# Kernel tuning notes

Measured on AMD Instinct MI355X. Metric: run time of the kernel, lower is better.

## Reference

```python
import jax, jax.numpy as jnp
import numpy as np

N_NODES = 50000
N_EDGES = 400000
N_GRAPHS = 32
EMB = 64
EDGE_DIM = 4
IN_DIM = 11
LAYERS = 4
EPS = 1e-5


def _bn(x, g, b):
    # BatchNorm1d in train mode: biased batch statistics over rows
    m = jnp.mean(x, axis=0)
    v = jnp.mean(jnp.square(x - m), axis=0)
    return g * (x - m) * jax.lax.rsqrt(v + EPS) + b


def setup_inputs() -> dict:
    key = jax.random.key(0)
    ks = jax.random.split(key, 16)
    x = jax.random.normal(ks[0], (N_NODES, IN_DIM), dtype=jnp.float32)
    edge_attr = jax.random.normal(ks[1], (N_EDGES, EDGE_DIM), dtype=jnp.float32)
    edge_index = jax.random.randint(ks[2], (2, N_EDGES), 0, N_NODES, dtype=jnp.int32)
    batch = jnp.sort(jax.random.randint(ks[3], (N_NODES,), 0, N_GRAPHS, dtype=jnp.int32))

    def lin(k, fan_in, shape):
        bound = 1.0 / np.sqrt(fan_in)
        return jax.random.uniform(k, shape, jnp.float32, -bound, bound)

    msg_in = 2 * EMB + EDGE_DIM  # 132
    upd_in = 2 * EMB             # 128
    kk = jax.random.split(ks[4], 12)
    params = dict(
        lin_in_W=lin(kk[0], IN_DIM, (IN_DIM, EMB)),
        lin_in_b=lin(kk[1], IN_DIM, (EMB,)),
        msg_W1=lin(kk[2], msg_in, (LAYERS, msg_in, EMB)),
        msg_b1=lin(kk[3], msg_in, (LAYERS, EMB)),
        msg_g1=jnp.ones((LAYERS, EMB), jnp.float32),
        msg_be1=jnp.zeros((LAYERS, EMB), jnp.float32),
        msg_W2=lin(kk[4], EMB, (LAYERS, EMB, EMB)),
        msg_b2=lin(kk[5], EMB, (LAYERS, EMB)),
        msg_g2=jnp.ones((LAYERS, EMB), jnp.float32),
        msg_be2=jnp.zeros((LAYERS, EMB), jnp.float32),
        upd_W1=lin(kk[6], upd_in, (LAYERS, upd_in, EMB)),
        upd_b1=lin(kk[7], upd_in, (LAYERS, EMB)),
        upd_g1=jnp.ones((LAYERS, EMB), jnp.float32),
        upd_be1=jnp.zeros((LAYERS, EMB), jnp.float32),
        upd_W2=lin(kk[8], EMB, (LAYERS, EMB, EMB)),
        upd_b2=lin(kk[9], EMB, (LAYERS, EMB)),
        upd_g2=jnp.ones((LAYERS, EMB), jnp.float32),
        upd_be2=jnp.zeros((LAYERS, EMB), jnp.float32),
        pred_W=lin(kk[10], EMB, (EMB, 1)),
        pred_b=lin(kk[11], EMB, (1,)),
    )
    return dict(x=x, edge_attr=edge_attr, edge_index=edge_index, batch=batch, **params)


def reference(x, edge_attr, edge_index, batch, lin_in_W, lin_in_b,
              msg_W1, msg_b1, msg_g1, msg_be1, msg_W2, msg_b2, msg_g2, msg_be2,
              upd_W1, upd_b1, upd_g1, upd_be1, upd_W2, upd_b2, upd_g2, upd_be2,
              pred_W, pred_b):
    src = edge_index[0]  # j (source)
    dst = edge_index[1]  # i (target, PyG default flow source_to_target)
    h = x @ lin_in_W + lin_in_b  # (n, d)
    for l in range(LAYERS):
        m_in = jnp.concatenate([h[dst], h[src], edge_attr], axis=-1)  # (e, 2d+d_e)
        m = jax.nn.relu(_bn(m_in @ msg_W1[l] + msg_b1[l], msg_g1[l], msg_be1[l]))
        m = jax.nn.relu(_bn(m @ msg_W2[l] + msg_b2[l], msg_g2[l], msg_be2[l]))
        aggr = jax.ops.segment_sum(m, dst, num_segments=N_NODES)  # scatter-add
        u_in = jnp.concatenate([h, aggr], axis=-1)  # (n, 2d)
        u = jax.nn.relu(_bn(u_in @ upd_W1[l] + upd_b1[l], upd_g1[l], upd_be1[l]))
        u = jax.nn.relu(_bn(u @ upd_W2[l] + upd_b2[l], upd_g2[l], upd_be2[l]))
        h = h + u  # residual in MPNNModel.forward
    sums = jax.ops.segment_sum(h, batch, num_segments=N_GRAPHS)
    counts = jax.ops.segment_sum(jnp.ones((h.shape[0],), h.dtype), batch, num_segments=N_GRAPHS)
    h_graph = sums / jnp.maximum(counts, 1.0)[:, None]  # global_mean_pool
    out = h_graph @ pred_W + pred_b  # (G, 1)
    return out.reshape(-1)
```

## Files before the change

kernel.cpp:

```cpp
#include <hip/hip_runtime.h>

#define DEV __device__ __forceinline__

constexpr int NN = 50000;
constexpr int NE = 400000;
constexpr int NG = 32;
constexpr float EPSV = 1e-5f;
constexpr int SCAN_BLOCKS = 196;
constexpr int NSHARD = 8;
constexpr int STB = NSHARD * 128;

typedef __attribute__((ext_vector_type(8))) short s16x8;
typedef __attribute__((ext_vector_type(4))) float f32x4;

DEV unsigned short f2b(float f) {
  union { float f; unsigned u; } x; x.f = f;
  unsigned r = x.u + 0x7fffu + ((x.u >> 16) & 1u);
  return (unsigned short)(r >> 16);
}
DEV float b2f(unsigned short u) {
  union { unsigned u; float f; } x; x.u = ((unsigned)u) << 16; return x.f;
}

DEV s16x8 frag_from_f32(const float* p) {
  const float4 v0 = *(const float4*)p;
  const float4 v1 = *(const float4*)(p + 4);
  s16x8 af;
  af[0] = (short)f2b(v0.x); af[1] = (short)f2b(v0.y);
  af[2] = (short)f2b(v0.z); af[3] = (short)f2b(v0.w);
  af[4] = (short)f2b(v1.x); af[5] = (short)f2b(v1.y);
  af[6] = (short)f2b(v1.z); af[7] = (short)f2b(v1.w);
  return af;
}

DEV void bn_coeff(const float* __restrict__ st, const float* __restrict__ g,
                  const float* __restrict__ be, float invM, int c,
                  float& sc, float& sh) {
  float s = 0.f, s2 = 0.f;
#pragma unroll
  for (int k = 0; k < NSHARD; ++k) {
    s += st[k * 128 + c];
    s2 += st[k * 128 + 64 + c];
  }
  float mean = s * invM;
  float var = s2 * invM - mean * mean;
  sc = g[c] * rsqrtf(var + EPSV);
  sh = be[c] - mean * sc;
}

__global__ __launch_bounds__(256) void lin_in_kernel(
    const float* __restrict__ x, const float* __restrict__ W,
    const float* __restrict__ b, float* __restrict__ h)
{
  int gid = blockIdx.x * 256 + threadIdx.x;
  if (gid >= NN * 64) return;
  int n = gid >> 6, c = gid & 63;
  float acc = b[c];
#pragma unroll
  for (int k = 0; k < 11; ++k)
    acc = fmaf(x[n * 11 + k], W[k * 64 + c], acc);
  h[gid] = acc;
}

__global__ __launch_bounds__(256) void hist_kernel(
    const int* __restrict__ dstI, int* __restrict__ deg)
{
  int e = blockIdx.x * 256 + threadIdx.x;
  if (e < NE) atomicAdd(&deg[dstI[e]], 1);
}

__global__ __launch_bounds__(256) void scan_pass1(
    const int* __restrict__ deg, int* __restrict__ blockSums)
{
  __shared__ int red[4];
  int tid = threadIdx.x;
  int idx = blockIdx.x * 256 + tid;
  int v = (idx < NN) ? deg[idx] : 0;
#pragma unroll
  for (int off = 32; off > 0; off >>= 1) v += __shfl_down(v, off, 64);
  if ((tid & 63) == 0) red[tid >> 6] = v;
  __syncthreads();
  if (tid == 0) blockSums[blockIdx.x] = red[0] + red[1] + red[2] + red[3];
}

__global__ __launch_bounds__(256) void scan_pass2(
    const int* __restrict__ blockSums, int* __restrict__ blockOffs)
{
  __shared__ int part[256];
  int tid = threadIdx.x;
  int v = (tid < SCAN_BLOCKS) ? blockSums[tid] : 0;
  part[tid] = v;
  __syncthreads();
  for (int off = 1; off < 256; off <<= 1) {
    int t = 0;
    if (tid >= off) t = part[tid - off];
    __syncthreads();
    if (tid >= off) part[tid] += t;
    __syncthreads();
  }
  blockOffs[tid] = (tid == 0) ? 0 : part[tid - 1];
}

__global__ __launch_bounds__(256) void scan_pass3(
    const int* __restrict__ deg, const int* __restrict__ blockOffs,
    int* __restrict__ rowptr, int* __restrict__ cursor)
{
  __shared__ int part[256];
  int tid = threadIdx.x;
  int idx = blockIdx.x * 256 + tid;
  int v = (idx < NN) ? deg[idx] : 0;
  part[tid] = v;
  __syncthreads();
  for (int off = 1; off < 256; off <<= 1) {
    int t = 0;
    if (tid >= off) t = part[tid - off];
    __syncthreads();
    if (tid >= off) part[tid] += t;
    __syncthreads();
  }
  int excl = (tid == 0) ? 0 : part[tid - 1];
  int val = blockOffs[blockIdx.x] + excl;
  if (idx < NN) { rowptr[idx] = val; cursor[idx] = val; }
  if (idx == 0) rowptr[NN] = NE;
}

__global__ __launch_bounds__(256) void fill_pos_kernel(
    const int* __restrict__ dstI, int* __restrict__ cursor,
    int* __restrict__ eid)
{
  int e = blockIdx.x * 256 + threadIdx.x;
  if (e < NE) {
    int pos = atomicAdd(&cursor[dstI[e]], 1);
    eid[pos] = e;
  }
}

__global__ __launch_bounds__(256) void permute_kernel(
    const int* __restrict__ eid, const int* __restrict__ srcI,
    const int* __restrict__ dstI, const float* __restrict__ ea,
    int* __restrict__ srcP, int* __restrict__ dstP,
    float* __restrict__ eaP)
{
  int p = blockIdx.x * 256 + threadIdx.x;
  if (p < NE) {
    int e = eid[p];
    srcP[p] = srcI[e];
    dstP[p] = dstI[e];
    *(float4*)&eaP[(size_t)p * 4] = *(const float4*)&ea[(size_t)e * 4];
  }
}

__global__ __launch_bounds__(256) void gemm_dual_mfma(
    const float* __restrict__ h, const float* __restrict__ W,
    unsigned short* __restrict__ Hd, unsigned short* __restrict__ Hs)
{
  __shared__ __align__(16) unsigned short Wt_s[2 * 64 * 72];

  const int tid = threadIdx.x;
  const int lane = tid & 63;
  const int wave = tid >> 6;
  const int nn = lane & 15;
  const int kq = lane >> 4;

#pragma unroll
  for (int i = 0; i < 32; ++i) {
    int idx = i * 256 + tid;
    int half = idx >> 12;
    int rem = idx & 4095;
    int k = rem >> 6, n = rem & 63;
    Wt_s[half * 4608 + n * 72 + k] = f2b(W[idx]);
  }
  __syncthreads();

  s16x8 bfrag[2][4][2];
#pragma unroll
  for (int o = 0; o < 2; ++o)
#pragma unroll
    for (int nt = 0; nt < 4; ++nt)
#pragma unroll
      for (int kc = 0; kc < 2; ++kc) {
        const unsigned short* p =
            &Wt_s[o * 4608 + (nt * 16 + nn) * 72 + kc * 32 + kq * 8];
#pragma unroll
        for (int j = 0; j < 8; ++j) bfrag[o][nt][kc][j] = (short)p[j];
      }

  const int rbase = blockIdx.x * 128 + wave * 32;

  f32x4 acc[2][2][4];
#pragma unroll
  for (int o = 0; o < 2; ++o)
#pragma unroll
    for (int rt = 0; rt < 2; ++rt)
#pragma unroll
      for (int nt = 0; nt < 4; ++nt) acc[o][rt][nt] = (f32x4){0.f, 0.f, 0.f, 0.f};

#pragma unroll
  for (int rt = 0; rt < 2; ++rt) {
    int row = rbase + rt * 16 + nn;
    int rowc = row < NN ? row : NN - 1;
#pragma unroll
    for (int kc = 0; kc < 2; ++kc) {
      s16x8 af = frag_from_f32(&h[(size_t)rowc * 64 + kc * 32 + kq * 8]);
#pragma unroll
      for (int o = 0; o < 2; ++o)
#pragma unroll
        for (int nt = 0; nt < 4; ++nt)
          acc[o][rt][nt] = __builtin_amdgcn_mfma_f32_16x16x32_bf16(
              af, bfrag[o][nt][kc], acc[o][rt][nt], 0, 0, 0);
    }
  }

#pragma unroll
  for (int rt = 0; rt < 2; ++rt)
#pragma unroll
    for (int nt = 0; nt < 4; ++nt) {
      int col = nt * 16 + nn;
#pragma unroll
      for (int reg = 0; reg < 4; ++reg) {
        int row = rbase + rt * 16 + kq * 4 + reg;
        if (row < NN) {
          Hd[(size_t)row * 64 + col] = f2b(acc[0][rt][nt][reg]);
          Hs[(size_t)row * 64 + col] = f2b(acc[1][rt][nt][reg]);
        }
      }
    }
}

__global__ __launch_bounds__(256) void edge_combine(
    const unsigned short* __restrict__ Hd, const unsigned short* __restrict__ Hs,
    const float* __restrict__ eaP, const int* __restrict__ srcP,
    const int* __restrict__ dstP, const float* __restrict__ Wb,
    const float* __restrict__ bias, unsigned short* __restrict__ t1,
    float* __restrict__ outStats)
{
  __shared__ float red_s[128];
  const int tid = threadIdx.x;
  const int c0 = (tid & 7) * 8;
  float bv[8], w0[8], w1[8], w2[8], w3[8];
#pragma unroll
  for (int j = 0; j < 8; ++j) {
    bv[j] = bias[c0 + j];
    w0[j] = Wb[0 * 64 + c0 + j];
    w1[j] = Wb[1 * 64 + c0 + j];
    w2[j] = Wb[2 * 64 + c0 + j];
    w3[j] = Wb[3 * 64 + c0 + j];
  }

  float s[8], s2[8];
#pragma unroll
  for (int j = 0; j < 8; ++j) { s[j] = 0.f; s2[j] = 0.f; }

  const int e0 = (blockIdx.x * 256 + tid) >> 3;
  const int estep = (gridDim.x * 256) >> 3;

  for (int e = e0; e < NE; e += 4 * estep) {
    bool has[4];
    uint4 hd[4], hs[4];
    float4 av[4];
    int eidx4[4];
#pragma unroll
    for (int u = 0; u < 4; ++u) {
      int ee = e + u * estep;
      has[u] = ee < NE;
      int ec = has[u] ? ee : e;
      eidx4[u] = ec;
      int si = srcP[ec], di = dstP[ec];
      av[u] = *(const float4*)&eaP[(size_t)ec * 4];
      hd[u] = *(const uint4*)&Hd[(size_t)di * 64 + c0];
      hs[u] = *(const uint4*)&Hs[(size_t)si * 64 + c0];
    }
#pragma unroll
    for (int u = 0; u < 4; ++u) {
      if (!has[u]) continue;
      const unsigned hdw[4] = {hd[u].x, hd[u].y, hd[u].z, hd[u].w};
      const unsigned hsw[4] = {hs[u].x, hs[u].y, hs[u].z, hs[u].w};
      unsigned short ob[8];
#pragma unroll
      for (int d = 0; d < 4; ++d) {
        union { unsigned uu; float f; } a0, a1, b0, b1u;
        a0.uu = (hdw[d] & 0xffffu) << 16; a1.uu = hdw[d] & 0xffff0000u;
        b0.uu = (hsw[d] & 0xffffu) << 16; b1u.uu = hsw[d] & 0xffff0000u;
        int j0 = d * 2, j1 = d * 2 + 1;
        float y0 = a0.f + b0.f + bv[j0] + av[u].x * w0[j0] + av[u].y * w1[j0] + av[u].z * w2[j0] + av[u].w * w3[j0];
        float y1 = a1.f + b1u.f + bv[j1] + av[u].x * w0[j1] + av[u].y * w1[j1] + av[u].z * w2[j1] + av[u].w * w3[j1];
        ob[j0] = f2b(y0); ob[j1] = f2b(y1);
        s[j0] += y0; s2[j0] += y0 * y0;
        s[j1] += y1; s2[j1] += y1 * y1;
      }
      *(uint4*)&t1[(size_t)eidx4[u] * 64 + c0] = *(const uint4*)ob;
    }
  }
#pragma unroll
  for (int j = 0; j < 8; ++j) {
    s[j] += __shfl_xor(s[j], 8, 64);
    s[j] += __shfl_xor(s[j], 16, 64);
    s[j] += __shfl_xor(s[j], 32, 64);
    s2[j] += __shfl_xor(s2[j], 8, 64);
    s2[j] += __shfl_xor(s2[j], 16, 64);
    s2[j] += __shfl_xor(s2[j], 32, 64);
  }
  if (tid < 128) red_s[tid] = 0.f;
  __syncthreads();
  if ((tid & 63) < 8) {
#pragma unroll
    for (int j = 0; j < 8; ++j) {
      atomicAdd(&red_s[c0 + j], s[j]);
      atomicAdd(&red_s[64 + c0 + j], s2[j]);
    }
  }
  __syncthreads();
  if (tid < 128)
    atomicAdd(&outStats[(blockIdx.x & (NSHARD - 1)) * 128 + tid], red_s[tid]);
}

__global__ __launch_bounds__(256) void gemm64_bn_mfma(
    const unsigned short* A0,
    const float* __restrict__ W,
    const float* __restrict__ bias,
    const float* __restrict__ inStats,
    const float* __restrict__ inG,
    const float* __restrict__ inBe,
    float invM_in,
    unsigned short* outp,
    float* __restrict__ outStats,
    int M)
{
  __shared__ __align__(16) unsigned short Wt_s[64 * 72];
  __shared__ float scale_s[64];
  __shared__ float shift_s[64];
  __shared__ float red_s[128];

  const int tid = threadIdx.x;
  const int lane = tid & 63;
  const int wave = tid >> 6;
  const int nn = lane & 15;
  const int kq = lane >> 4;

  if (tid < 64) {
    float sc, sh;
    bn_coeff(inStats, inG, inBe, invM_in, tid, sc, sh);
    scale_s[tid] = sc;
    shift_s[tid] = sh;
  }
#pragma unroll
  for (int i = 0; i < 16; ++i) {
    int idx = i * 256 + tid;
    int k = idx >> 6, n = idx & 63;
    Wt_s[n * 72 + k] = f2b(W[idx]);
  }
  __syncthreads();

  s16x8 bfrag[4][2];
#pragma unroll
  for (int nt = 0; nt < 4; ++nt)
#pragma unroll
    for (int kc = 0; kc < 2; ++kc)
      bfrag[nt][kc] = *(const s16x8*)&Wt_s[(nt * 16 + nn) * 72 + kc * 32 + kq * 8];

  float scf[2][8], shf[2][8];
#pragma unroll
  for (int kc = 0; kc < 2; ++kc) {
    int k0 = kc * 32 + kq * 8;
    float4 a = *(const float4*)&scale_s[k0];
    float4 b = *(const float4*)&scale_s[k0 + 4];
    float4 c = *(const float4*)&shift_s[k0];
    float4 d = *(const float4*)&shift_s[k0 + 4];
    scf[kc][0] = a.x; scf[kc][1] = a.y; scf[kc][2] = a.z; scf[kc][3] = a.w;
    scf[kc][4] = b.x; scf[kc][5] = b.y; scf[kc][6] = b.z; scf[kc][7] = b.w;
    shf[kc][0] = c.x; shf[kc][1] = c.y; shf[kc][2] = c.z; shf[kc][3] = c.w;
    shf[kc][4] = d.x; shf[kc][5] = d.y; shf[kc][6] = d.z; shf[kc][7] = d.w;
  }

  float bcol[4];
#pragma unroll
  for (int nt = 0; nt < 4; ++nt) bcol[nt] = bias[nt * 16 + nn];

  float s[4] = {0.f, 0.f, 0.f, 0.f};
  float s2[4] = {0.f, 0.f, 0.f, 0.f};

  uint4 raw[4][2];
  f32x4 acc[4][4];

  const int rb0 = blockIdx.x * 512 + wave * 64;
#pragma unroll
  for (int rt = 0; rt < 4; ++rt) {
    int row = rb0 + rt * 16 + nn;
    int rowc = row < M ? row : M - 1;
#pragma unroll
    for (int kc = 0; kc < 2; ++kc)
      raw[rt][kc] = *(const uint4*)&A0[(size_t)rowc * 64 + kc * 32 + kq * 8];
  }

#pragma unroll
  for (int rt = 0; rt < 4; ++rt)
#pragma unroll
    for (int nt = 0; nt < 4; ++nt) acc[rt][nt] = (f32x4){0.f, 0.f, 0.f, 0.f};
#pragma unroll
  for (int rt = 0; rt < 4; ++rt) {
#pragma unroll
    for (int kc = 0; kc < 2; ++kc) {
      unsigned wbits[4] = {raw[rt][kc].x, raw[rt][kc].y, raw[rt][kc].z, raw[rt][kc].w};
      s16x8 af;
#pragma unroll
      for (int d = 0; d < 4; ++d) {
        union { unsigned u; float f; } lo, hi;
        lo.u = (wbits[d] & 0xffffu) << 16;
        hi.u = wbits[d] & 0xffff0000u;
        int j0 = d * 2, j1 = d * 2 + 1;
        af[j0] = (short)f2b(fmaxf(fmaf(scf[kc][j0], lo.f, shf[kc][j0]), 0.f));
        af[j1] = (short)f2b(fmaxf(fmaf(scf[kc][j1], hi.f, shf[kc][j1]), 0.f));
      }
#pragma unroll
      for (int nt = 0; nt < 4; ++nt)
        acc[rt][nt] = __builtin_amdgcn_mfma_f32_16x16x32_bf16(
            af, bfrag[nt][kc], acc[rt][nt], 0, 0, 0);
    }
  }

  const int rb1 = rb0 + 256;
#pragma unroll
  for (int rt = 0; rt < 4; ++rt) {
    int row = rb1 + rt * 16 + nn;
    int rowc = row < M ? row : M - 1;
#pragma unroll
    for (int kc = 0; kc < 2; ++kc)
      raw[rt][kc] = *(const uint4*)&A0[(size_t)rowc * 64 + kc * 32 + kq * 8];
  }

#pragma unroll
  for (int rt = 0; rt < 4; ++rt)
#pragma unroll
    for (int nt = 0; nt < 4; ++nt) {
      int col = nt * 16 + nn;
#pragma unroll
      for (int reg = 0; reg < 4; ++reg) {
        int row = rb0 + rt * 16 + kq * 4 + reg;
        if (row < M) {
          float y = acc[rt][nt][reg] + bcol[nt];
          outp[(size_t)row * 64 + col] = f2b(y);
          s[nt] += y; s2[nt] += y * y;
        }
      }
    }

#pragma unroll
  for (int rt = 0; rt < 4; ++rt)
#pragma unroll
    for (int nt = 0; nt < 4; ++nt) acc[rt][nt] = (f32x4){0.f, 0.f, 0.f, 0.f};
#pragma unroll
  for (int rt = 0; rt < 4; ++rt) {
#pragma unroll
    for (int kc = 0; kc < 2; ++kc) {
      unsigned wbits[4] = {raw[rt][kc].x, raw[rt][kc].y, raw[rt][kc].z, raw[rt][kc].w};
      s16x8 af;
#pragma unroll
      for (int d = 0; d < 4; ++d) {
        union { unsigned u; float f; } lo, hi;
        lo.u = (wbits[d] & 0xffffu) << 16;
        hi.u = wbits[d] & 0xffff0000u;
        int j0 = d * 2, j1 = d * 2 + 1;
        af[j0] = (short)f2b(fmaxf(fmaf(scf[kc][j0], lo.f, shf[kc][j0]), 0.f));
        af[j1] = (short)f2b(fmaxf(fmaf(scf[kc][j1], hi.f, shf[kc][j1]), 0.f));
      }
#pragma unroll
      for (int nt = 0; nt < 4; ++nt)
        acc[rt][nt] = __builtin_amdgcn_mfma_f32_16x16x32_bf16(
            af, bfrag[nt][kc], acc[rt][nt], 0, 0, 0);
    }
  }

#pragma unroll
  for (int rt = 0; rt < 4; ++rt)
#pragma unroll
    for (int nt = 0; nt < 4; ++nt) {
      int col = nt * 16 + nn;
#pragma unroll
      for (int reg = 0; reg < 4; ++reg) {
        int row = rb1 + rt * 16 + kq * 4 + reg;
        if (row < M) {
          float y = acc[rt][nt][reg] + bcol[nt];
          outp[(size_t)row * 64 + col] = f2b(y);
          s[nt] += y; s2[nt] += y * y;
        }
      }
    }

#pragma unroll
  for (int nt = 0; nt < 4; ++nt) {
    s[nt] += __shfl_xor(s[nt], 16, 64);
    s[nt] += __shfl_xor(s[nt], 32, 64);
    s2[nt] += __shfl_xor(s2[nt], 16, 64);
    s2[nt] += __shfl_xor(s2[nt], 32, 64);
  }
  if (tid < 128) red_s[tid] = 0.f;
  __syncthreads();
  if (lane < 16) {
#pragma unroll
    for (int nt = 0; nt < 4; ++nt) {
      atomicAdd(&red_s[nt * 16 + nn], s[nt]);
      atomicAdd(&red_s[64 + nt * 16 + nn], s2[nt]);
    }
  }
  __syncthreads();
  if (tid < 128)
    atomicAdd(&outStats[(blockIdx.x & (NSHARD - 1)) * 128 + tid], red_s[tid]);
}

__global__ __launch_bounds__(256) void gemm_concat_mfma(
    const float* __restrict__ A0,
    const unsigned short* __restrict__ A1b,
    const float* __restrict__ W,
    const float* __restrict__ bias,
    unsigned short* __restrict__ outp,
    float* __restrict__ outStats,
    int M)
{
  __shared__ __align__(16) unsigned short Wt_s[64 * 136];
  __shared__ float red_s[128];

  const int tid = threadIdx.x;
  const int lane = tid & 63;
  const int wave = tid >> 6;
  const int nn = lane & 15;
  const int kq = lane >> 4;

#pragma unroll
  for (int i = 0; i < 32; ++i) {
    int idx = i * 256 + tid;
    int k = idx >> 6, n = idx & 63;
    Wt_s[n * 136 + k] = f2b(W[idx]);
  }
  __syncthreads();

  s16x8 bfrag[4][4];
#pragma unroll
  for (int nt = 0; nt < 4; ++nt)
#pragma unroll
    for (int kc = 0; kc < 4; ++kc) {
      const unsigned short* p = &Wt_s[(nt * 16 + nn) * 136 + kc * 32 + kq * 8];
#pragma unroll
      for (int j = 0; j < 8; ++j) bfrag[nt][kc][j] = (short)p[j];
    }

  const int rbase = blockIdx.x * 128 + wave * 32;

  f32x4 acc[2][4];
#pragma unroll
  for (int rt = 0; rt < 2; ++rt)
#pragma unroll
    for (int nt = 0; nt < 4; ++nt) acc[rt][nt] = (f32x4){0.f, 0.f, 0.f, 0.f};

#pragma unroll
  for (int rt = 0; rt < 2; ++rt) {
    int row = rbase + rt * 16 + nn;
    int rowc = row < M ? row : M - 1;
#pragma unroll
    for (int kc = 0; kc < 4; ++kc) {
      s16x8 af;
      if (kc < 2) {
        af = frag_from_f32(&A0[(size_t)rowc * 64 + kc * 32 + kq * 8]);
      } else {
        af = *(const s16x8*)&A1b[(size_t)rowc * 64 + (kc - 2) * 32 + kq * 8];
      }
#pragma unroll
      for (int nt = 0; nt < 4; ++nt)
        acc[rt][nt] = __builtin_amdgcn_mfma_f32_16x16x32_bf16(
            af, bfrag[nt][kc], acc[rt][nt], 0, 0, 0);
    }
  }

  float bcol[4];
#pragma unroll
  for (int nt = 0; nt < 4; ++nt) bcol[nt] = bias[nt * 16 + nn];

  float s[4] = {0.f, 0.f, 0.f, 0.f};
  float s2[4] = {0.f, 0.f, 0.f, 0.f};
#pragma unroll
  for (int rt = 0; rt < 2; ++rt)
#pragma unroll
    for (int nt = 0; nt < 4; ++nt) {
      int col = nt * 16 + nn;
#pragma unroll
      for (int reg = 0; reg < 4; ++reg) {
        int row = rbase + rt * 16 + kq * 4 + reg;
        if (row < M) {
          float y = acc[rt][nt][reg] + bcol[nt];
          outp[(size_t)row * 64 + col] = f2b(y);
          s[nt] += y; s2[nt] += y * y;
        }
      }
    }
#pragma unroll
  for (int nt = 0; nt < 4; ++nt) {
    s[nt] += __shfl_xor(s[nt], 16, 64);
    s[nt] += __shfl_xor(s[nt], 32, 64);
    s2[nt] += __shfl_xor(s2[nt], 16, 64);
    s2[nt] += __shfl_xor(s2[nt], 32, 64);
  }
  if (tid < 128) red_s[tid] = 0.f;
  __syncthreads();
  if (lane < 16) {
#pragma unroll
    for (int nt = 0; nt < 4; ++nt) {
      atomicAdd(&red_s[nt * 16 + nn], s[nt]);
      atomicAdd(&red_s[64 + nt * 16 + nn], s2[nt]);
    }
  }
  __syncthreads();
  if (tid < 128)
    atomicAdd(&outStats[(blockIdx.x & (NSHARD - 1)) * 128 + tid], red_s[tid]);
}

__global__ __launch_bounds__(256) void aggregate_kernel(
    const unsigned short* __restrict__ t2, const int* __restrict__ rowptr,
    const float* __restrict__ stats, const float* __restrict__ g,
    const float* __restrict__ be, float invM,
    unsigned short* __restrict__ aggr)
{
  __shared__ float sc_s[64], sh_s[64];
  const int tid = threadIdx.x;
  if (tid < 64) {
    float sc, sh;
    bn_coeff(stats, g, be, invM, tid, sc, sh);
    sc_s[tid] = sc;
    sh_s[tid] = sh;
  }
  __syncthreads();

  int node = (blockIdx.x * 256 + tid) >> 6;
  int lane = tid & 63;
  if (node >= NN) return;
  const int c8 = (lane & 7) * 8;
  const int rq = lane >> 3;

  float sc[8], sh[8];
#pragma unroll
  for (int j = 0; j < 8; ++j) {
    sc[j] = sc_s[c8 + j];
    sh[j] = sh_s[c8 + j];
  }

  int lo = rowptr[node], hi = rowptr[node + 1];
  float acc[8] = {0.f, 0.f, 0.f, 0.f, 0.f, 0.f, 0.f, 0.f};

  for (int i = lo; i < hi; i += 16) {
    int r0 = i + rq;
    int r1 = i + 8 + rq;
    bool h0 = r0 < hi, h1 = r1 < hi;
    uint4 v0 = make_uint4(0u, 0u, 0u, 0u), v1 = make_uint4(0u, 0u, 0u, 0u);
    if (h0) v0 = *(const uint4*)&t2[(size_t)r0 * 64 + c8];
    if (h1) v1 = *(const uint4*)&t2[(size_t)r1 * 64 + c8];
    if (h0) {
      const unsigned w[4] = {v0.x, v0.y, v0.z, v0.w};
#pragma unroll
      for (int d = 0; d < 4; ++d) {
        union { unsigned u; float f; } a0, a1;
        a0.u = (w[d] & 0xffffu) << 16;
        a1.u = w[d] & 0xffff0000u;
        acc[d * 2] += fmaxf(fmaf(sc[d * 2], a0.f, sh[d * 2]), 0.f);
        acc[d * 2 + 1] += fmaxf(fmaf(sc[d * 2 + 1], a1.f, sh[d * 2 + 1]), 0.f);
      }
    }
    if (h1) {
      const unsigned w[4] = {v1.x, v1.y, v1.z, v1.w};
#pragma unroll
      for (int d = 0; d < 4; ++d) {
        union { unsigned u; float f; } a0, a1;
        a0.u = (w[d] & 0xffffu) << 16;
        a1.u = w[d] & 0xffff0000u;
        acc[d * 2] += fmaxf(fmaf(sc[d * 2], a0.f, sh[d * 2]), 0.f);
        acc[d * 2 + 1] += fmaxf(fmaf(sc[d * 2 + 1], a1.f, sh[d * 2 + 1]), 0.f);
      }
    }
  }
#pragma unroll
  for (int j = 0; j < 8; ++j) {
    acc[j] += __shfl_xor(acc[j], 8, 64);
    acc[j] += __shfl_xor(acc[j], 16, 64);
    acc[j] += __shfl_xor(acc[j], 32, 64);
  }
  if (rq == 0) {
    unsigned short o[8];
#pragma unroll
    for (int j = 0; j < 8; ++j) o[j] = f2b(acc[j]);
    *(uint4*)&aggr[(size_t)node * 64 + c8] = *(const uint4*)o;
  }
}

__global__ __launch_bounds__(256) void residual_kernel(
    const unsigned short* __restrict__ u2, const float* __restrict__ stats,
    const float* __restrict__ g, const float* __restrict__ be,
    float invM, float* __restrict__ h)
{
  __shared__ float sc_s[64], sh_s[64];
  const int tid = threadIdx.x;
  if (tid < 64) {
    float sc, sh;
    bn_coeff(stats, g, be, invM, tid, sc, sh);
    sc_s[tid] = sc;
    sh_s[tid] = sh;
  }
  __syncthreads();

  int gid = blockIdx.x * 256 + tid;
  if (gid >= NN * 16) return;
  int c = (gid & 15) * 4;
  ushort4 v4 = *(const ushort4*)&u2[(size_t)gid * 4];
  float4 hv = *(const float4*)&h[(size_t)gid * 4];
  const unsigned short vu[4] = {v4.x, v4.y, v4.z, v4.w};
  float* hp = (float*)&hv;
#pragma unroll
  for (int j = 0; j < 4; ++j)
    hp[j] += fmaxf(fmaf(sc_s[c + j], b2f(vu[j]), sh_s[c + j]), 0.f);
  *(float4*)&h[(size_t)gid * 4] = hv;
}

constexpr int POOL_NPB = 128;

__global__ __launch_bounds__(256) void pool_partial(
    const float* __restrict__ h, const int* __restrict__ batch,
    float* __restrict__ sums)
{
  int lane = threadIdx.x & 63;
  int wave = threadIdx.x >> 6;
  int base = blockIdx.x * POOL_NPB;
  float acc = 0.f;
  int gcur = -1;
  for (int i = wave; i < POOL_NPB; i += 4) {
    int n = base + i;
    if (n >= NN) break;
    int g = batch[n];
    if (g != gcur) {
      if (gcur >= 0) atomicAdd(&sums[gcur * 64 + lane], acc);
      gcur = g;
      acc = 0.f;
    }
    acc += h[(size_t)n * 64 + lane];
  }
  if (gcur >= 0) atomicAdd(&sums[gcur * 64 + lane], acc);
}

DEV int lower_bound_i(const int* __restrict__ a, int n, int v) {
  int lo = 0, hi = n;
  while (lo < hi) {
    int m = (lo + hi) >> 1;
    if (a[m] < v) lo = m + 1; else hi = m;
  }
  return lo;
}

__global__ __launch_bounds__(64) void pool_final(
    const float* __restrict__ sums, const int* __restrict__ batch,
    const float* __restrict__ predW, const float* __restrict__ predB,
    float* __restrict__ out)
{
  int g = blockIdx.x;
  int lane = threadIdx.x;
  int lo = lower_bound_i(batch, NN, g);
  int hi = lower_bound_i(batch, NN, g + 1);
  float cnt = fmaxf((float)(hi - lo), 1.0f);
  float p = sums[g * 64 + lane] / cnt * predW[lane];
#pragma unroll
  for (int off = 32; off > 0; off >>= 1) p += __shfl_down(p, off, 64);
  if (lane == 0) out[g] = p + predB[0];
}

extern "C" void kernel_launch(void* const* d_in, const int* in_sizes, int n_in,
                              void* d_out, int out_size, void* d_ws, size_t ws_size,
                              hipStream_t stream)
{
  (void)in_sizes; (void)n_in; (void)out_size; (void)ws_size;

  const float* x        = (const float*)d_in[0];
  const float* edge_attr= (const float*)d_in[1];
  const int*   eidx     = (const int*)d_in[2];
  const int*   batch    = (const int*)d_in[3];
  const float* linW     = (const float*)d_in[4];
  const float* linB     = (const float*)d_in[5];
  const float* msgW1    = (const float*)d_in[6];
  const float* msgB1    = (const float*)d_in[7];
  const float* msgG1    = (const float*)d_in[8];
  const float* msgBe1   = (const float*)d_in[9];
  const float* msgW2    = (const float*)d_in[10];
  const float* msgB2    = (const float*)d_in[11];
  const float* msgG2    = (const float*)d_in[12];
  const float* msgBe2   = (const float*)d_in[13];
  const float* updW1    = (const float*)d_in[14];
  const float* updB1    = (const float*)d_in[15];
  const float* updG1    = (const float*)d_in[16];
  const float* updBe1   = (const float*)d_in[17];
  const float* updW2    = (const float*)d_in[18];
  const float* updB2    = (const float*)d_in[19];
  const float* updG2    = (const float*)d_in[20];
  const float* updBe2   = (const float*)d_in[21];
  const float* predW    = (const float*)d_in[22];
  const float* predB    = (const float*)d_in[23];

  const int* srcI = eidx;
  const int* dstI = eidx + NE;

  char* p = (char*)d_ws;
  float* h  = (float*)p;            p += (size_t)NN * 64 * 4;
  unsigned short* t1 = (unsigned short*)p; p += (size_t)NE * 64 * 2;
  unsigned short* aggr = (unsigned short*)p; p += (size_t)NN * 64 * 2;
  unsigned short* u1 = (unsigned short*)p;   p += (size_t)NN * 64 * 2;
  unsigned short* Hd = (unsigned short*)p;   p += (size_t)NN * 64 * 2;
  unsigned short* Hs = (unsigned short*)p;   p += (size_t)NN * 64 * 2;
  float* stats = (float*)p;         p += 16 * STB * 4;
  float* sums = (float*)p;          p += NG * 64 * 4;
  int* deg = (int*)p;               p += (size_t)NN * 4;
  int* cursor = (int*)p;            p += (size_t)NN * 4;
  int* rowptr = (int*)p;            p += (size_t)(NN + 1) * 4;
  int* eid = (int*)p;               p += (size_t)NE * 4;
  int* srcP = (int*)p;              p += (size_t)NE * 4;
  int* dstP = (int*)p;              p += (size_t)NE * 4;
  float* eaP = (float*)p;           p += (size_t)NE * 4 * 4;
  int* blockSums = (int*)p;         p += 256 * 4;
  int* blockOffs = (int*)p;         p += 256 * 4;

  hipMemsetAsync(stats, 0, (16 * STB + NG * 64) * sizeof(float), stream);
  hipMemsetAsync(deg, 0, NN * sizeof(int), stream);

  hist_kernel<<<(NE + 255) / 256, 256, 0, stream>>>(dstI, deg);
  scan_pass1<<<SCAN_BLOCKS, 256, 0, stream>>>(deg, blockSums);
  scan_pass2<<<1, 256, 0, stream>>>(blockSums, blockOffs);
  scan_pass3<<<SCAN_BLOCKS, 256, 0, stream>>>(deg, blockOffs, rowptr, cursor);
  fill_pos_kernel<<<(NE + 255) / 256, 256, 0, stream>>>(dstI, cursor, eid);
  permute_kernel<<<(NE + 255) / 256, 256, 0, stream>>>(
      eid, srcI, dstI, edge_attr, srcP, dstP, eaP);

  lin_in_kernel<<<(NN * 64 + 255) / 256, 256, 0, stream>>>(x, linW, linB, h);

  const float invE = 1.0f / (float)NE;
  const float invN = 1.0f / (float)NN;
  const int NB128 = (NN + 127) / 128;
  const int NB512 = (NN + 511) / 512;
  const int EB512 = (NE + 511) / 512;

  for (int l = 0; l < 4; ++l) {
    float* st0 = stats + (l * 4 + 0) * STB;
    float* st1 = stats + (l * 4 + 1) * STB;
    float* st2 = stats + (l * 4 + 2) * STB;
    float* st3 = stats + (l * 4 + 3) * STB;
    const float* W1 = msgW1 + (size_t)l * 132 * 64;

    gemm_dual_mfma<<<NB128, 256, 0, stream>>>(h, W1, Hd, Hs);

    edge_combine<<<2048, 256, 0, stream>>>(
        Hd, Hs, eaP, srcP, dstP, W1 + 128 * 64, msgB1 + l * 64,
        t1, st0);

    gemm64_bn_mfma<<<EB512, 256, 0, stream>>>(
        t1, msgW2 + (size_t)l * 64 * 64, msgB2 + l * 64,
        st0, msgG1 + l * 64, msgBe1 + l * 64, invE,
        t1, st1, NE);

    aggregate_kernel<<<(NN * 64 + 255) / 256, 256, 0, stream>>>(
        t1, rowptr, st1, msgG2 + l * 64, msgBe2 + l * 64, invE, aggr);

    gemm_concat_mfma<<<NB128, 256, 0, stream>>>(
        h, aggr, updW1 + (size_t)l * 128 * 64, updB1 + l * 64,
        u1, st2, NN);

    gemm64_bn_mfma<<<NB512, 256, 0, stream>>>(
        u1, updW2 + (size_t)l * 64 * 64, updB2 + l * 64,
        st2, updG1 + l * 64, updBe1 + l * 64, invN,
        u1, st3, NN);

    residual_kernel<<<(NN * 16 + 255) / 256, 256, 0, stream>>>(
        u1, st3, updG2 + l * 64, updBe2 + l * 64, invN, h);
  }

  pool_partial<<<(NN + POOL_NPB - 1) / POOL_NPB, 256, 0, stream>>>(h, batch, sums);
  pool_final<<<NG, 64, 0, stream>>>(sums, batch, predW, predB, (float*)d_out);
}
```

Before: 661.3 us.

## Fuse neighbor aggregation into the update concat GEMM kernel

Aggregation of BN+ReLU edge messages per node now runs inside the update-MLP first GEMM, writing each block's aggregated rows to shared memory instead of a global buffer. This removes one kernel launch and the global write/read of the aggregate tensor. Each wave now serially processes 32 nodes two at a time, which greatly reduces parallelism for the gather phase and may expose memory latency. The B-fragment loads from LDS are also vectorized.

```diff
diff --git a/kernel.cpp b/kernel.cpp
--- a/kernel.cpp
+++ b/kernel.cpp
@@ -507,9 +507,11 @@
     atomicAdd(&outStats[(blockIdx.x & (NSHARD - 1)) * 128 + tid], red_s[tid]);
 }
 
-__global__ __launch_bounds__(256) void gemm_concat_mfma(
-    const float* __restrict__ A0,
-    const unsigned short* __restrict__ A1b,
+__global__ __launch_bounds__(256) void aggr_concat_mfma(
+    const unsigned short* __restrict__ t2, const int* __restrict__ rowptr,
+    const float* __restrict__ st1, const float* __restrict__ g2,
+    const float* __restrict__ be2, float invE,
+    const float* __restrict__ h,
     const float* __restrict__ W,
     const float* __restrict__ bias,
     unsigned short* __restrict__ outp,
@@ -517,6 +519,8 @@
     int M)
 {
   __shared__ __align__(16) unsigned short Wt_s[64 * 136];
+  __shared__ __align__(16) unsigned short A2_s[128 * 72];
+  __shared__ float sc_s[64], sh_s[64];
   __shared__ float red_s[128];
 
   const int tid = threadIdx.x;
@@ -525,6 +529,12 @@
   const int nn = lane & 15;
   const int kq = lane >> 4;
 
+  if (tid < 64) {
+    float sc, sh;
+    bn_coeff(st1, g2, be2, invE, tid, sc, sh);
+    sc_s[tid] = sc;
+    sh_s[tid] = sh;
+  }
 #pragma unroll
   for (int i = 0; i < 32; ++i) {
     int idx = i * 256 + tid;
@@ -533,15 +543,76 @@
   }
   __syncthreads();
 
+  {
+    const int c8 = (lane & 7) * 8;
+    const int rq = lane >> 3;
+    float sc[8], sh[8];
+#pragma unroll
+    for (int j = 0; j < 8; ++j) { sc[j] = sc_s[c8 + j]; sh[j] = sh_s[c8 + j]; }
+
+    const int nodeBase = blockIdx.x * 128 + wave * 32;
+    for (int i = 0; i < 32; i += 2) {
+      int nA = nodeBase + i, nB = nodeBase + i + 1;
+      int loA = 0, hiA = 0, loB = 0, hiB = 0;
+      if (nA < NN) { loA = rowptr[nA]; hiA = rowptr[nA + 1]; }
+      if (nB < NN) { loB = rowptr[nB]; hiB = rowptr[nB + 1]; }
+      float accA[8] = {0.f, 0.f, 0.f, 0.f, 0.f, 0.f, 0.f, 0.f};
+      float accB[8] = {0.f, 0.f, 0.f, 0.f, 0.f, 0.f, 0.f, 0.f};
+      int iA = loA + rq, iB = loB + rq;
+      while (iA < hiA || iB < hiB) {
+        bool hA = iA < hiA, hB = iB < hiB;
+        uint4 vA = make_uint4(0u, 0u, 0u, 0u), vB = make_uint4(0u, 0u, 0u, 0u);
+        if (hA) vA = *(const uint4*)&t2[(size_t)iA * 64 + c8];
+        if (hB) vB = *(const uint4*)&t2[(size_t)iB * 64 + c8];
+        if (hA) {
+          const unsigned w[4] = {vA.x, vA.y, vA.z, vA.w};
+#pragma unroll
+          for (int d = 0; d < 4; ++d) {
+            union { unsigned u; float f; } a0, a1;
+            a0.u = (w[d] & 0xffffu) << 16;
+            a1.u = w[d] & 0xffff0000u;
+            accA[d * 2] += fmaxf(fmaf(sc[d * 2], a0.f, sh[d * 2]), 0.f);
+            accA[d * 2 + 1] += fmaxf(fmaf(sc[d * 2 + 1], a1.f, sh[d * 2 + 1]), 0.f);
+          }
+        }
+        if (hB) {
+          const unsigned w[4] = {vB.x, vB.y, vB.z, vB.w};
+#pragma unroll
+          for (int d = 0; d < 4; ++d) {
+            union { unsigned u; float f; } a0, a1;
+            a0.u = (w[d] & 0xffffu) << 16;
+            a1.u = w[d] & 0xffff0000u;
+            accB[d * 2] += fmaxf(fmaf(sc[d * 2], a0.f, sh[d * 2]), 0.f);
+            accB[d * 2 + 1] += fmaxf(fmaf(sc[d * 2 + 1], a1.f, sh[d * 2 + 1]), 0.f);
+          }
+        }
+        iA += 8; iB += 8;
+      }
+#pragma unroll
+      for (int j = 0; j < 8; ++j) {
+        accA[j] += __shfl_xor(accA[j], 8, 64);
+        accA[j] += __shfl_xor(accA[j], 16, 64);
+        accA[j] += __shfl_xor(accA[j], 32, 64);
+        accB[j] += __shfl_xor(accB[j], 8, 64);
+        accB[j] += __shfl_xor(accB[j], 16, 64);
+        accB[j] += __shfl_xor(accB[j], 32, 64);
+      }
+      if (rq == 0) {
+        unsigned short oA[8], oB[8];
+#pragma unroll
+        for (int j = 0; j < 8; ++j) { oA[j] = f2b(accA[j]); oB[j] = f2b(accB[j]); }
+        *(uint4*)&A2_s[(wave * 32 + i) * 72 + c8] = *(const uint4*)oA;
+        *(uint4*)&A2_s[(wave * 32 + i + 1) * 72 + c8] = *(const uint4*)oB;
+      }
+    }
+  }
+
   s16x8 bfrag[4][4];
 #pragma unroll
   for (int nt = 0; nt < 4; ++nt)
 #pragma unroll
-    for (int kc = 0; kc < 4; ++kc) {
-      const unsigned short* p = &Wt_s[(nt * 16 + nn) * 136 + kc * 32 + kq * 8];
-#pragma unroll
-      for (int j = 0; j < 8; ++j) bfrag[nt][kc][j] = (short)p[j];
-    }
+    for (int kc = 0; kc < 4; ++kc)
+      bfrag[nt][kc] = *(const s16x8*)&Wt_s[(nt * 16 + nn) * 136 + kc * 32 + kq * 8];
 
   const int rbase = blockIdx.x * 128 + wave * 32;
 
@@ -555,13 +626,14 @@
   for (int rt = 0; rt < 2; ++rt) {
     int row = rbase + rt * 16 + nn;
     int rowc = row < M ? row : M - 1;
+    int rloc = wave * 32 + rt * 16 + nn;
 #pragma unroll
     for (int kc = 0; kc < 4; ++kc) {
       s16x8 af;
       if (kc < 2) {
-        af = frag_from_f32(&A0[(size_t)rowc * 64 + kc * 32 + kq * 8]);
+        af = frag_from_f32(&h[(size_t)rowc * 64 + kc * 32 + kq * 8]);
       } else {
-        af = *(const s16x8*)&A1b[(size_t)rowc * 64 + (kc - 2) * 32 + kq * 8];
+        af = *(const s16x8*)&A2_s[rloc * 72 + (kc - 2) * 32 + kq * 8];
       }
 #pragma unroll
       for (int nt = 0; nt < 4; ++nt)
@@ -610,82 +682,6 @@
   __syncthreads();
   if (tid < 128)
     atomicAdd(&outStats[(blockIdx.x & (NSHARD - 1)) * 128 + tid], red_s[tid]);
-}
-
-__global__ __launch_bounds__(256) void aggregate_kernel(
-    const unsigned short* __restrict__ t2, const int* __restrict__ rowptr,
-    const float* __restrict__ stats, const float* __restrict__ g,
-    const float* __restrict__ be, float invM,
-    unsigned short* __restrict__ aggr)
-{
-  __shared__ float sc_s[64], sh_s[64];
-  const int tid = threadIdx.x;
-  if (tid < 64) {
-    float sc, sh;
-    bn_coeff(stats, g, be, invM, tid, sc, sh);
-    sc_s[tid] = sc;
-    sh_s[tid] = sh;
-  }
-  __syncthreads();
-
-  int node = (blockIdx.x * 256 + tid) >> 6;
-  int lane = tid & 63;
-  if (node >= NN) return;
-  const int c8 = (lane & 7) * 8;
-  const int rq = lane >> 3;
-
-  float sc[8], sh[8];
-#pragma unroll
-  for (int j = 0; j < 8; ++j) {
-    sc[j] = sc_s[c8 + j];
-    sh[j] = sh_s[c8 + j];
-  }
-
-  int lo = rowptr[node], hi = rowptr[node + 1];
-  float acc[8] = {0.f, 0.f, 0.f, 0.f, 0.f, 0.f, 0.f, 0.f};
-
-  for (int i = lo; i < hi; i += 16) {
-    int r0 = i + rq;
-    int r1 = i + 8 + rq;
-    bool h0 = r0 < hi, h1 = r1 < hi;
-    uint4 v0 = make_uint4(0u, 0u, 0u, 0u), v1 = make_uint4(0u, 0u, 0u, 0u);
-    if (h0) v0 = *(const uint4*)&t2[(size_t)r0 * 64 + c8];
-    if (h1) v1 = *(const uint4*)&t2[(size_t)r1 * 64 + c8];
-    if (h0) {
-      const unsigned w[4] = {v0.x, v0.y, v0.z, v0.w};
-#pragma unroll
-      for (int d = 0; d < 4; ++d) {
-        union { unsigned u; float f; } a0, a1;
-        a0.u = (w[d] & 0xffffu) << 16;
-        a1.u = w[d] & 0xffff0000u;
-        acc[d * 2] += fmaxf(fmaf(sc[d * 2], a0.f, sh[d * 2]), 0.f);
-        acc[d * 2 + 1] += fmaxf(fmaf(sc[d * 2 + 1], a1.f, sh[d * 2 + 1]), 0.f);
-      }
-    }
-    if (h1) {
-      const unsigned w[4] = {v1.x, v1.y, v1.z, v1.w};
-#pragma unroll
-      for (int d = 0; d < 4; ++d) {
-        union { unsigned u; float f; } a0, a1;
-        a0.u = (w[d] & 0xffffu) << 16;
-        a1.u = w[d] & 0xffff0000u;
-        acc[d * 2] += fmaxf(fmaf(sc[d * 2], a0.f, sh[d * 2]), 0.f);
-        acc[d * 2 + 1] += fmaxf(fmaf(sc[d * 2 + 1], a1.f, sh[d * 2 + 1]), 0.f);
-      }
-    }
-  }
-#pragma unroll
-  for (int j = 0; j < 8; ++j) {
-    acc[j] += __shfl_xor(acc[j], 8, 64);
-    acc[j] += __shfl_xor(acc[j], 16, 64);
-    acc[j] += __shfl_xor(acc[j], 32, 64);
-  }
-  if (rq == 0) {
-    unsigned short o[8];
-#pragma unroll
-    for (int j = 0; j < 8; ++j) o[j] = f2b(acc[j]);
-    *(uint4*)&aggr[(size_t)node * 64 + c8] = *(const uint4*)o;
-  }
 }
 
 __global__ __launch_bounds__(256) void residual_kernel(
@@ -803,7 +799,6 @@
   char* p = (char*)d_ws;
   float* h  = (float*)p;            p += (size_t)NN * 64 * 4;
   unsigned short* t1 = (unsigned short*)p; p += (size_t)NE * 64 * 2;
-  unsigned short* aggr = (unsigned short*)p; p += (size_t)NN * 64 * 2;
   unsigned short* u1 = (unsigned short*)p;   p += (size_t)NN * 64 * 2;
   unsigned short* Hd = (unsigned short*)p;   p += (size_t)NN * 64 * 2;
   unsigned short* Hs = (unsigned short*)p;   p += (size_t)NN * 64 * 2;
@@ -856,11 +851,9 @@
         st0, msgG1 + l * 64, msgBe1 + l * 64, invE,
         t1, st1, NE);
 
-    aggregate_kernel<<<(NN * 64 + 255) / 256, 256, 0, stream>>>(
-        t1, rowptr, st1, msgG2 + l * 64, msgBe2 + l * 64, invE, aggr);
-
-    gemm_concat_mfma<<<NB128, 256, 0, stream>>>(
-        h, aggr, updW1 + (size_t)l * 128 * 64, updB1 + l * 64,
+    aggr_concat_mfma<<<NB128, 256, 0, stream>>>(
+        t1, rowptr, st1, msgG2 + l * 64, msgBe2 + l * 64, invE,
+        h, updW1 + (size_t)l * 128 * 64, updB1 + l * 64,
         u1, st2, NN);
 
     gemm64_bn_mfma<<<NB512, 256, 0, stream>>>(
```

After: 702.5 us. +6.2%, slower.
